# Performance work log

Hardware: AMD Instinct MI355X
Metric: run time of the kernel (lower is better)

## Reference

```python
import jax, jax.numpy as jnp
import numpy as np

N_NODES = 100000
N_EDGES = 1600000
EMB = 128
N_LAYER = 5
X_DIM = 178
E_DIM = 18
BN_EPS = 1e-5


def setup_inputs() -> dict:
    key = jax.random.key(0)
    ks = jax.random.split(key, 20)
    s = 0.05  # weight scale
    inp = {}
    inp["x"] = jax.random.normal(ks[0], (N_NODES, X_DIM), jnp.float32)
    inp["edge_attr"] = jax.random.uniform(ks[1], (N_EDGES, E_DIM), jnp.float32)
    # input MLP (178 -> emb -> emb, LeakyReLU 0.1)
    inp["iw1"] = jax.random.normal(ks[2], (X_DIM, EMB), jnp.float32) * s
    inp["ib1"] = jax.random.normal(ks[3], (EMB,), jnp.float32) * s
    inp["iw2"] = jax.random.normal(ks[4], (EMB, EMB), jnp.float32) * s
    inp["ib2"] = jax.random.normal(ks[5], (EMB,), jnp.float32) * s
    # per-layer edge embedding MLP (18 -> emb -> emb, LeakyReLU 0.1)
    inp["ew1"] = jax.random.normal(ks[6], (N_LAYER, E_DIM, EMB), jnp.float32) * s
    inp["eb1"] = jax.random.normal(ks[7], (N_LAYER, EMB), jnp.float32) * s
    inp["ew2"] = jax.random.normal(ks[8], (N_LAYER, EMB, EMB), jnp.float32) * s
    inp["eb2"] = jax.random.normal(ks[9], (N_LAYER, EMB), jnp.float32) * s
    # per-layer GIN update MLP (emb -> 2emb -> emb, ReLU)
    inp["mw1"] = jax.random.normal(ks[10], (N_LAYER, EMB, 2 * EMB), jnp.float32) * s
    inp["mb1"] = jax.random.normal(ks[11], (N_LAYER, 2 * EMB), jnp.float32) * s
    inp["mw2"] = jax.random.normal(ks[12], (N_LAYER, 2 * EMB, EMB), jnp.float32) * s
    inp["mb2"] = jax.random.normal(ks[13], (N_LAYER, EMB), jnp.float32) * s
    # per-layer BatchNorm affine params
    inp["gamma"] = jnp.ones((N_LAYER, EMB), jnp.float32)
    inp["beta"] = jnp.zeros((N_LAYER, EMB), jnp.float32)
    inp["edge_index"] = jax.random.randint(ks[14], (2, N_EDGES), 0, N_NODES)
    return inp


def _leaky(v):
    return jnp.where(v > 0, v, 0.1 * v)


def reference(x, edge_attr, iw1, ib1, iw2, ib2, ew1, eb1, ew2, eb2,
              mw1, mb1, mw2, mb2, gamma, beta, edge_index):
    src = edge_index[0]  # x_j gathered from source nodes (PyG source_to_target)
    dst = edge_index[1]
    n = x.shape[0]

    # input node MLP with LeakyReLU(0.1)
    h = _leaky(x @ iw1 + ib1) @ iw2 + ib2  # [N, EMB]

    for l in range(N_LAYER):
        # edge embeddings for real edges: [E, EMB]
        ee = _leaky(edge_attr @ ew1[l] + eb1[l]) @ ew2[l] + eb2[l]
        # self-loop edges have zero edge_attr -> constant embedding vector [EMB]
        self_e = _leaky(eb1[l]) @ ew2[l] + eb2[l]
        # message = x_j + edge_emb; aggregate (add) at destination, plus self-loop term
        msg = h[src] + ee
        aggr = jax.ops.segment_sum(msg, dst, num_segments=n) + h + self_e
        # GIN update MLP (ReLU)
        hh = jnp.maximum(aggr @ mw1[l] + mb1[l], 0.0) @ mw2[l] + mb2[l]
        # BatchNorm1d (training mode: batch stats, biased variance)
        mean = hh.mean(axis=0)
        var = hh.var(axis=0)
        hh = (hh - mean) / jnp.sqrt(var + BN_EPS) * gamma[l] + beta[l]
        if l < N_LAYER - 1:
            hh = jnp.maximum(hh, 0.0)  # ReLU on all but last layer; dropout p=0 is a no-op
        h = hh

    return h  # JK == 'last'
```

## Files before the change

### kernel.cpp

```cpp
#include <hip/hip_runtime.h>
#include <hip/hip_bf16.h>
#include <cstdint>
#include <cstddef>

#define NNODES 100000
#define NEDGES 1600000
#define EMBD 128
#define NLAYER 5
#define XDIM 178
#define EDIM 18
#define BNEPS 1e-5f

typedef __attribute__((ext_vector_type(8))) short short8;
typedef __attribute__((ext_vector_type(8))) unsigned short ushort8;
typedef __attribute__((ext_vector_type(4))) float f32x4;

static __device__ __forceinline__ float leakyf(float v){ return v > 0.f ? v : 0.1f*v; }
static __device__ __forceinline__ unsigned short f2b(float v){
  __hip_bfloat16 b = __float2bfloat16(v);
  return *reinterpret_cast<unsigned short*>(&b);
}
static __device__ __forceinline__ float b2f(unsigned short u){
  __hip_bfloat16 b = *reinterpret_cast<__hip_bfloat16*>(&u);
  return __bfloat162float(b);
}

__global__ __launch_bounds__(256) void k_hist(const int* __restrict__ dst, int* __restrict__ cnt){
  int e = blockIdx.x*256 + threadIdx.x;
  if (e < NEDGES) atomicAdd(&cnt[dst[e]], 1);
}

__global__ __launch_bounds__(256) void k_scan1(const int* __restrict__ cnt, int* __restrict__ rowptr,
                                               int* __restrict__ bsum){
  __shared__ int s[256];
  int t = threadIdx.x, i = blockIdx.x*256 + t;
  int v = (i < NNODES) ? cnt[i] : 0;
  s[t] = v; __syncthreads();
  for (int off=1; off<256; off<<=1){
    int x = (t>=off) ? s[t-off] : 0; __syncthreads();
    s[t] += x; __syncthreads();
  }
  if (i < NNODES) rowptr[i+1] = s[t];
  if (t == 255) bsum[blockIdx.x] = s[t];
}

__global__ __launch_bounds__(512) void k_scan2(const int* __restrict__ bsum, int* __restrict__ boff, int nb){
  __shared__ int s[512];
  int t = threadIdx.x;
  int v = (t < nb) ? bsum[t] : 0;
  s[t] = v; __syncthreads();
  for (int off=1; off<512; off<<=1){
    int x = (t>=off) ? s[t-off] : 0; __syncthreads();
    s[t] += x; __syncthreads();
  }
  if (t < nb) boff[t] = s[t] - v;
}

__global__ __launch_bounds__(256) void k_scan3(int* __restrict__ rowptr, const int* __restrict__ boff){
  int i = blockIdx.x*256 + threadIdx.x;
  if (i < NNODES) rowptr[i+1] += boff[i>>8];
  if (i == 0) rowptr[0] = 0;
}

__global__ __launch_bounds__(256) void k_curcopy(const int* __restrict__ rowptr, int* __restrict__ cursor){
  int i = blockIdx.x*256 + threadIdx.x;
  if (i < NNODES) cursor[i] = rowptr[i];
}

__global__ __launch_bounds__(256) void k_fill_new(const int* __restrict__ src, const int* __restrict__ dst,
                                                  const float* __restrict__ ea, int* __restrict__ cursor,
                                                  int* __restrict__ srcp, unsigned short* __restrict__ eap24){
  int e = blockIdx.x*256 + threadIdx.x;
  if (e >= NEDGES) return;
  int pos = atomicAdd(&cursor[dst[e]], 1);
  srcp[pos] = src[e];
  const float* a = ea + (size_t)e*EDIM;
  ushort8 r0, r1, r2;
  #pragma unroll
  for (int k=0;k<8;++k)  r0[k] = f2b(a[k]);
  #pragma unroll
  for (int k=0;k<8;++k)  r1[k] = f2b(a[8+k]);
  #pragma unroll
  for (int k=0;k<8;++k)  r2[k] = 0;
  r2[0] = f2b(a[16]); r2[1] = f2b(a[17]);
  r2[2] = 0x3F80;
  unsigned short* o = eap24 + (size_t)pos*24;
  *reinterpret_cast<ushort8*>(o)      = r0;
  *reinterpret_cast<ushort8*>(o + 8)  = r1;
  *reinterpret_cast<ushort8*>(o + 16) = r2;
}

__global__ __launch_bounds__(256) void k_fill(const int* __restrict__ src, const int* __restrict__ dst,
                                              const float* __restrict__ ea, int* __restrict__ cursor,
                                              int* __restrict__ perm, int* __restrict__ srcp,
                                              float* __restrict__ eap){
  int e = blockIdx.x*256 + threadIdx.x;
  if (e >= NEDGES) return;
  int pos = atomicAdd(&cursor[dst[e]], 1);
  perm[pos] = e;
  srcp[pos] = src[e];
  if (eap){
    const float* a = ea + (size_t)e*EDIM;
    float* o = eap + (size_t)pos*EDIM;
    #pragma unroll
    for (int k=0;k<EDIM;++k) o[k] = a[k];
  }
}

__global__ __launch_bounds__(128) void k_selfe(const float* __restrict__ eb1, const float* __restrict__ ew2,
                                               const float* __restrict__ eb2, float* __restrict__ selfe){
  int l = blockIdx.x, c = threadIdx.x;
  const float* b1 = eb1 + l*EMBD;
  const float* w2 = ew2 + (size_t)l*EMBD*EMBD;
  float acc = eb2[l*EMBD + c];
  for (int j=0;j<EMBD;++j) acc += leakyf(b1[j]) * w2[j*EMBD + c];
  selfe[l*EMBD + c] = acc;
}

__global__ __launch_bounds__(256) void k_wc(const float* __restrict__ ew2, const float* __restrict__ mw1,
                                            float* __restrict__ wc){
  int idx = blockIdx.x*256 + threadIdx.x;
  int l = idx >> 15, rem = idx & 32767;
  int i = rem >> 8, n = rem & 255;
  const float* e = ew2 + (size_t)l*EMBD*EMBD + i*EMBD;
  const float* m = mw1 + (size_t)l*EMBD*2*EMBD + n;
  float acc = 0.f;
  #pragma unroll 4
  for (int j=0;j<EMBD;++j) acc += e[j]*m[(size_t)j*2*EMBD];
  wc[idx] = acc;
}

__global__ __launch_bounds__(256) void k_pack(const float* __restrict__ s1, int rows1,
                                              const float* __restrict__ s2, int Kreal,
                                              int Kpad, int N, __hip_bfloat16* __restrict__ out){
  int idx = blockIdx.x*256 + threadIdx.x;
  if (idx >= Kpad*N) return;
  int k = idx / N, n = idx - k*N;
  float v = 0.f;
  if (k < rows1) v = s1[(size_t)k*N + n];
  else if (k < Kreal) v = s2[(size_t)(k-rows1)*N + n];
  unsigned short hi = f2b(v);
  unsigned short lo = f2b(v - b2f(hi));
  size_t o = (size_t)(k>>5)*N*32 + (size_t)n*32 + (k&31);
  unsigned short* po = (unsigned short*)out;
  po[o] = hi;
  po[(size_t)Kpad*N + o] = lo;
}

__global__ __launch_bounds__(256) void k_gather(
    const float* __restrict__ h, const int* __restrict__ rowptr,
    const int* __restrict__ srcp,
    const float* __restrict__ eb2l, const float* __restrict__ selfel,
    float* __restrict__ base)
{
  int tid = threadIdx.x;
  int li = tid & 31;
  int c4 = li*4;
  float4 sf4 = *(const float4*)(selfel + c4);
  float4 e24 = *(const float4*)(eb2l + c4);
  int slot = blockIdx.x*8 + (tid>>5);
  const int NS = gridDim.x*8;
  for (int node = slot; node < NNODES; node += NS){
    int rs = rowptr[node], re = rowptr[node+1];
    f32x4 b = (f32x4)0.f;
    for (int c0 = rs; c0 < re; c0 += 8){
      int cnt = re - c0;
      #pragma unroll
      for (int p=0;p<8;++p){
        int e = c0 + p; if (e > re-1) e = re-1;
        float m = (p < cnt) ? 1.f : 0.f;
        int sp = srcp[e];
        float4 hv = *(const float4*)(h + (size_t)sp*EMBD + c4);
        b[0] = fmaf(m, hv.x, b[0]);
        b[1] = fmaf(m, hv.y, b[1]);
        b[2] = fmaf(m, hv.z, b[2]);
        b[3] = fmaf(m, hv.w, b[3]);
      }
    }
    float deg = (float)(re - rs);
    float4 hn = *(const float4*)(h + (size_t)node*EMBD + c4);
    float4 o;
    o.x = b[0] + hn.x + sf4.x + deg*e24.x;
    o.y = b[1] + hn.y + sf4.y + deg*e24.y;
    o.z = b[2] + hn.z + sf4.z + deg*e24.z;
    o.w = b[3] + hn.w + sf4.w + deg*e24.w;
    *(float4*)(base + (size_t)node*EMBD + c4) = o;
  }
}

__global__ __launch_bounds__(256) void k_s1(
    const int* __restrict__ rowptr, const unsigned short* __restrict__ eap24,
    const float* __restrict__ ew1l, const float* __restrict__ eb1l,
    float* __restrict__ S1)
{
  int tid = threadIdx.x;
  int lane = tid & 63;
  int lr = lane & 15, kb = lane >> 4;

  short8 bh[8], bl[8];
  #pragma unroll
  for (int nf=0; nf<8; ++nf){
    int col = nf*16 + lr;
    ushort8 hh8, ll8;
    #pragma unroll
    for (int j=0;j<8;++j){
      int k = kb*8 + j;
      float v = 0.f;
      if (k < EDIM) v = ew1l[k*EMBD + col];
      else if (k == EDIM) v = eb1l[col];
      unsigned short hi = f2b(v);
      hh8[j] = hi;
      ll8[j] = f2b(v - b2f(hi));
    }
    bh[nf] = *reinterpret_cast<short8*>(&hh8);
    bl[nf] = *reinterpret_cast<short8*>(&ll8);
  }

  int wid = blockIdx.x*4 + (tid>>6);
  const int NW = gridDim.x*4;
  for (int node = wid; node < NNODES; node += NW){
    int rs = rowptr[node], re = rowptr[node+1];
    float s1p[8];
    #pragma unroll
    for (int nf=0;nf<8;++nf) s1p[nf]=0.f;

    for (int c0 = rs; c0 < re; c0 += 16){
      int cnt = re - c0;
      int idx = c0 + lr; if (idx > re-1) idx = re-1;
      short8 af = (short8)0;
      if (kb < 3){
        ushort8 t = *reinterpret_cast<const ushort8*>(eap24 + (size_t)idx*24 + kb*8);
        af = *reinterpret_cast<short8*>(&t);
      }
      if (lr >= cnt) af = (short8)0;
      #pragma unroll
      for (int nf=0;nf<8;++nf){
        f32x4 acc = (f32x4)0.f;
        acc = __builtin_amdgcn_mfma_f32_16x16x32_bf16(af, bl[nf], acc, 0,0,0);
        acc = __builtin_amdgcn_mfma_f32_16x16x32_bf16(af, bh[nf], acc, 0,0,0);
        #pragma unroll
        for (int j=0;j<4;++j){
          float v = acc[j];
          s1p[nf] = fmaf(0.55f, v, s1p[nf]);
          s1p[nf] = fmaf(0.45f, fabsf(v), s1p[nf]);
        }
      }
    }

    #pragma unroll
    for (int nf=0;nf<8;++nf){
      float v = s1p[nf];
      v += __shfl_xor(v, 16);
      v += __shfl_xor(v, 32);
      s1p[nf] = v;
    }
    float va = s1p[0], vb = s1p[1];
    if (kb == 1){ va = s1p[2]; vb = s1p[3]; }
    if (kb == 2){ va = s1p[4]; vb = s1p[5]; }
    if (kb == 3){ va = s1p[6]; vb = s1p[7]; }
    S1[(size_t)node*EMBD + kb*32 + lr]      = va;
    S1[(size_t)node*EMBD + kb*32 + 16 + lr] = vb;
  }
}

__global__ __launch_bounds__(256) void k_edge(
    const float* __restrict__ h, const int* __restrict__ rowptr,
    const int* __restrict__ perm, const int* __restrict__ srcp,
    const float* __restrict__ edge_attr, const float* __restrict__ eaperm,
    const float* __restrict__ ew1l, const float* __restrict__ eb1l,
    const float* __restrict__ eb2l, const float* __restrict__ selfel,
    float* __restrict__ S1, float* __restrict__ base)
{
  __shared__ float w1s[EDIM*EMBD];
  __shared__ float b1s[EMBD];
  int tid = threadIdx.x;
  for (int i = tid; i < EDIM*EMBD; i += 256) w1s[i] = ew1l[i];
  if (tid < EMBD) b1s[tid] = eb1l[tid];
  __syncthreads();
  int lane = tid & 63;
  int node = blockIdx.x*4 + (tid >> 6);
  if (node >= NNODES) return;
  int rs = rowptr[node], re = rowptr[node+1];
  int c0 = lane*2;
  float s1x=0.f, s1y=0.f, bx=0.f, by=0.f;
  for (int i = rs; i < re; ++i){
    int s = __builtin_amdgcn_readfirstlane(srcp[i]);
    const float* ea;
    if (eaperm){
      ea = eaperm + (size_t)__builtin_amdgcn_readfirstlane(i)*EDIM;
    } else {
      ea = edge_attr + (size_t)__builtin_amdgcn_readfirstlane(perm[i])*EDIM;
    }
    float2 hs = *(const float2*)(h + (size_t)s*EMBD + c0);
    bx += hs.x; by += hs.y;
    float d0 = b1s[c0], d1 = b1s[c0+1];
    #pragma unroll
    for (int k=0;k<EDIM;++k){
      float av = ea[k];
      d0 += av * w1s[k*EMBD + c0];
      d1 += av * w1s[k*EMBD + c0 + 1];
    }
    s1x += leakyf(d0); s1y += leakyf(d1);
  }
  float deg = (float)(re - rs);
  float2 hv = *(const float2*)(h + (size_t)node*EMBD + c0);
  *(float2*)(S1 + (size_t)node*EMBD + c0) = make_float2(s1x, s1y);
  float bvx = bx + hv.x + selfel[c0]   + deg*eb2l[c0];
  float bvy = by + hv.y + selfel[c0+1] + deg*eb2l[c0+1];
  *(float2*)(base + (size_t)node*EMBD + c0) = make_float2(bvx, bvy);
}

template<int BN, int WGM, int WGN, bool ALO, int ACT, bool STATS, bool OBF16, bool CONCAT, bool KCHK, bool ABF16>
__global__ __launch_bounds__(512) void k_mgemm(
    const float* __restrict__ Af, const float* __restrict__ A1,
    const __hip_bfloat16* __restrict__ Ab,
    int M, int Kreal, int Kpad, int lda,
    const __hip_bfloat16* __restrict__ Bp,
    const float* __restrict__ bias,
    float* __restrict__ Cf, __hip_bfloat16* __restrict__ Cb, int ldc,
    float* __restrict__ stats)
{
  static_assert(WGM*WGN == 8, "8 waves");
  constexpr int BM = 128;
  constexpr int MF = BM/(16*WGM);
  constexpr int NF = BN/(16*WGN);
  constexpr int LDS_ROW = 40;
  __shared__ __align__(16) unsigned short Ah[BM*LDS_ROW];
  __shared__ __align__(16) unsigned short Al[ALO ? BM*LDS_ROW : 8];
  __shared__ float ssum[STATS ? BN : 4];
  __shared__ float ssq [STATS ? BN : 4];

  int tid = threadIdx.x;
  int row0 = blockIdx.x*BM;
  int w = tid >> 6, lane = tid & 63;
  int wm = w / WGN, wn = w % WGN;
  int lr = lane & 15, kb = lane >> 4;
  int wrow = wm*MF*16, wcol = wn*NF*16;

  if (STATS && tid < BN){ ssum[tid] = 0.f; ssq[tid] = 0.f; }

  f32x4 acc[MF][NF];
  #pragma unroll
  for (int a=0;a<MF;++a)
    #pragma unroll
    for (int b=0;b<NF;++b) acc[a][b] = (f32x4)0.f;

  const size_t planeSz = (size_t)Kpad*BN;
  int sr = tid >> 2;
  int skq = (tid & 3)*8;
  int grow = row0 + sr;
  const int KS = Kpad >> 5;

  for (int ks = 0; ks < KS; ++ks){
    int k0 = ks << 5;
    int kg = k0 + skq;
    ushort8 hv, lv;
    if (ABF16){
      short8 raw = (short8)0;
      if (grow < M) raw = *reinterpret_cast<const short8*>((const unsigned short*)Ab + (size_t)grow*lda + kg);
      hv = *reinterpret_cast<ushort8*>(&raw);
    } else {
      float v[8];
      if (KCHK){
        #pragma unroll
        for (int i=0;i<8;++i)
          v[i] = (grow < M && kg+i < Kreal) ? Af[(size_t)grow*lda + kg + i] : 0.f;
      } else {
        const float* s;
        if (CONCAT) s = (kg < EMBD) ? (Af + (size_t)grow*lda + kg) : (A1 + (size_t)grow*lda + (kg - EMBD));
        else        s = Af + (size_t)grow*lda + kg;
        float4 p0 = make_float4(0,0,0,0), p1 = make_float4(0,0,0,0);
        if (grow < M){ p0 = *(const float4*)s; p1 = *(const float4*)(s+4); }
        v[0]=p0.x; v[1]=p0.y; v[2]=p0.z; v[3]=p0.w;
        v[4]=p1.x; v[5]=p1.y; v[6]=p1.z; v[7]=p1.w;
      }
      #pragma unroll
      for (int i=0;i<8;++i){
        unsigned short h16 = f2b(v[i]);
        hv[i] = h16;
        if (ALO) lv[i] = f2b(v[i] - b2f(h16));
      }
    }
    __syncthreads();
    *reinterpret_cast<ushort8*>(&Ah[sr*LDS_ROW + skq]) = hv;
    if (ALO && !ABF16) *reinterpret_cast<ushort8*>(&Al[sr*LDS_ROW + skq]) = lv;
    __syncthreads();

    short8 ah[MF], al[MF];
    #pragma unroll
    for (int mf=0; mf<MF; ++mf){
      int r = (wrow + mf*16 + lr)*LDS_ROW + kb*8;
      ah[mf] = *reinterpret_cast<const short8*>(&Ah[r]);
      if (ALO) al[mf] = *reinterpret_cast<const short8*>(&Al[r]);
    }
    const unsigned short* bb = (const unsigned short*)Bp + (size_t)ks*BN*32;
    short8 bh[NF], blv[NF];
    #pragma unroll
    for (int nf=0; nf<NF; ++nf){
      size_t off = (size_t)(wcol + nf*16 + lr)*32 + kb*8;
      bh[nf] = *reinterpret_cast<const short8*>(bb + off);
      blv[nf] = *reinterpret_cast<const short8*>(bb + planeSz + off);
    }
    #pragma unroll
    for (int mf=0; mf<MF; ++mf){
      #pragma unroll
      for (int nf=0; nf<NF; ++nf){
        acc[mf][nf] = __builtin_amdgcn_mfma_f32_16x16x32_bf16(ah[mf], bh[nf], acc[mf][nf], 0, 0, 0);
        acc[mf][nf] = __builtin_amdgcn_mfma_f32_16x16x32_bf16(ah[mf], blv[nf], acc[mf][nf], 0, 0, 0);
        if (ALO)
          acc[mf][nf] = __builtin_amdgcn_mfma_f32_16x16x32_bf16(al[mf], bh[nf], acc[mf][nf], 0, 0, 0);
      }
    }
  }

  float bcol[NF];
  #pragma unroll
  for (int nf=0; nf<NF; ++nf) bcol[nf] = bias ? bias[wcol + nf*16 + lr] : 0.f;
  float s[NF], sq[NF];
  #pragma unroll
  for (int nf=0; nf<NF; ++nf){ s[nf]=0.f; sq[nf]=0.f; }

  #pragma unroll
  for (int mf=0; mf<MF; ++mf){
    #pragma unroll
    for (int j=0; j<4; ++j){
      int r = row0 + wrow + mf*16 + kb*4 + j;
      if (r < M){
        #pragma unroll
        for (int nf=0; nf<NF; ++nf){
          int c = wcol + nf*16 + lr;
          float v = acc[mf][nf][j] + bcol[nf];
          if (ACT == 1) v = leakyf(v);
          if (ACT == 2) v = fmaxf(v, 0.f);
          if (OBF16) Cb[(size_t)r*ldc + c] = __float2bfloat16(v);
          else       Cf[(size_t)r*ldc + c] = v;
          if (STATS){ s[nf] += v; sq[nf] += v*v; }
        }
      }
    }
  }
  if (STATS){
    #pragma unroll
    for (int nf=0; nf<NF; ++nf){
      atomicAdd(&ssum[wcol + nf*16 + lr], s[nf]);
      atomicAdd(&ssq [wcol + nf*16 + lr], sq[nf]);
    }
    __syncthreads();
    if (tid < BN){
      atomicAdd(&stats[tid], ssum[tid]);
      atomicAdd(&stats[BN + tid], ssq[tid]);
    }
  }
}

__global__ __launch_bounds__(256) void k_bn(const float* __restrict__ hh, const float* __restrict__ stats,
                                            const float* __restrict__ gamma, const float* __restrict__ beta,
                                            float* __restrict__ out, int dorelu){
  int idx = blockIdx.x*256 + threadIdx.x;
  if (idx >= NNODES*(EMBD/4)) return;
  int c0 = (idx & (EMBD/4 - 1)) * 4;
  float4 v = *(const float4*)(hh + (size_t)idx*4);
  float o[4] = {v.x, v.y, v.z, v.w};
  const float invN = 1.f / (float)NNODES;
  #pragma unroll
  for (int i=0;i<4;++i){
    int c = c0 + i;
    float mean = stats[c] * invN;
    float var  = stats[EMBD + c] * invN - mean*mean;
    float inv  = rsqrtf(fmaxf(var, 0.f) + BNEPS);
    float y = (o[i] - mean) * inv * gamma[c] + beta[c];
    if (dorelu) y = fmaxf(y, 0.f);
    o[i] = y;
  }
  *(float4*)(out + (size_t)idx*4) = make_float4(o[0],o[1],o[2],o[3]);
}

extern "C" void kernel_launch(void* const* d_in, const int* in_sizes, int n_in,
                              void* d_out, int out_size, void* d_ws, size_t ws_size,
                              hipStream_t stream)
{
  const float* x   = (const float*)d_in[0];
  const float* ea  = (const float*)d_in[1];
  const float* iw1 = (const float*)d_in[2];
  const float* ib1 = (const float*)d_in[3];
  const float* iw2 = (const float*)d_in[4];
  const float* ib2 = (const float*)d_in[5];
  const float* ew1 = (const float*)d_in[6];
  const float* eb1 = (const float*)d_in[7];
  const float* ew2 = (const float*)d_in[8];
  const float* eb2 = (const float*)d_in[9];
  const float* mw1 = (const float*)d_in[10];
  const float* mb1 = (const float*)d_in[11];
  const float* mw2 = (const float*)d_in[12];
  const float* mb2 = (const float*)d_in[13];
  const float* gamma = (const float*)d_in[14];
  const float* beta  = (const float*)d_in[15];
  const int* eidx = (const int*)d_in[16];
  const int* srcI = eidx;
  const int* dstI = eidx + NEDGES;

  char* p = (char*)d_ws;
  auto alloc = [&](size_t bytes)->char*{
    char* r = p; p += (bytes + 255) & ~(size_t)255; return r;
  };
  float* hbuf  = (float*)alloc((size_t)NNODES*EMBD*4);
  float* S1    = (float*)alloc((size_t)NNODES*EMBD*4);
  float* base  = (float*)alloc((size_t)NNODES*EMBD*4);
  __hip_bfloat16* tbuf = (__hip_bfloat16*)alloc((size_t)NNODES*2*EMBD*2);
  int* perm   = (int*)alloc((size_t)NEDGES*4);
  int* srcp   = (int*)alloc((size_t)NEDGES*4);
  int* rowptr = (int*)alloc((size_t)(NNODES+1)*4);
  int* cursor = (int*)alloc((size_t)NNODES*4);
  int* bsum   = (int*)alloc(4096);
  int* boff   = (int*)alloc(4096);
  float* selfe = (float*)alloc(NLAYER*EMBD*4);
  float* stats = (float*)alloc(2*EMBD*4);
  float* wc    = (float*)alloc((size_t)NLAYER*EMBD*2*EMBD*4);
  __hip_bfloat16* Bi1 = (__hip_bfloat16*)alloc((size_t)192*EMBD*2*2);
  __hip_bfloat16* Bi2 = (__hip_bfloat16*)alloc((size_t)EMBD*EMBD*2*2);
  __hip_bfloat16* B1  = (__hip_bfloat16*)alloc((size_t)NLAYER*256*256*2*2);
  __hip_bfloat16* B2  = (__hip_bfloat16*)alloc((size_t)NLAYER*256*EMBD*2*2);
  size_t used = (size_t)(p - (char*)d_ws);

  bool use_new = (ws_size >= used + (size_t)NEDGES*24*2 + 256);
  unsigned short* eap24 = nullptr;
  float* eaperm = nullptr;
  if (use_new) eap24 = (unsigned short*)alloc((size_t)NEDGES*24*2);
  else if (ws_size >= used + (size_t)NEDGES*EDIM*4 + 256)
    eaperm = (float*)alloc((size_t)NEDGES*EDIM*4);

  hipMemsetAsync(cursor, 0, (size_t)NNODES*4, stream);
  k_hist<<<(NEDGES+255)/256, 256, 0, stream>>>(dstI, cursor);
  int nb = (NNODES+255)/256;
  k_scan1<<<nb, 256, 0, stream>>>(cursor, rowptr, bsum);
  k_scan2<<<1, 512, 0, stream>>>(bsum, boff, nb);
  k_scan3<<<(NNODES+255)/256, 256, 0, stream>>>(rowptr, boff);
  k_curcopy<<<(NNODES+255)/256, 256, 0, stream>>>(rowptr, cursor);
  if (use_new)
    k_fill_new<<<(NEDGES+255)/256, 256, 0, stream>>>(srcI, dstI, ea, cursor, srcp, eap24);
  else
    k_fill<<<(NEDGES+255)/256, 256, 0, stream>>>(srcI, dstI, ea, cursor, perm, srcp, eaperm);
  k_selfe<<<NLAYER, EMBD, 0, stream>>>(eb1, ew2, eb2, selfe);

  k_wc<<<(NLAYER*EMBD*2*EMBD)/256, 256, 0, stream>>>(ew2, mw1, wc);
  k_pack<<<(192*EMBD+255)/256, 256, 0, stream>>>(iw1, XDIM, iw1, XDIM, 192, EMBD, Bi1);
  k_pack<<<(EMBD*EMBD+255)/256, 256, 0, stream>>>(iw2, EMBD, iw2, EMBD, EMBD, EMBD, Bi2);
  for (int l=0; l<NLAYER; ++l){
    k_pack<<<(256*256+255)/256, 256, 0, stream>>>(
        wc + (size_t)l*EMBD*2*EMBD, EMBD, mw1 + (size_t)l*EMBD*2*EMBD, 256, 256, 256,
        B1 + (size_t)l*256*256*2);
    k_pack<<<(256*EMBD+255)/256, 256, 0, stream>>>(
        mw2 + (size_t)l*2*EMBD*EMBD, 256, mw2, 256, 256, EMBD,
        B2 + (size_t)l*256*EMBD*2);
  }

  const int gx = (NNODES + 127)/128;

  k_mgemm<128,4,2, true,1,false,false,false,true ,false><<<gx, 512, 0, stream>>>(
      x, nullptr, nullptr, NNODES, XDIM, 192, XDIM, Bi1, ib1, S1, nullptr, EMBD, nullptr);
  k_mgemm<128,4,2, true,0,false,false,false,false,false><<<gx, 512, 0, stream>>>(
      S1, nullptr, nullptr, NNODES, EMBD, EMBD, EMBD, Bi2, ib2, hbuf, nullptr, EMBD, nullptr);

  for (int l=0; l<NLAYER; ++l){
    hipMemsetAsync(stats, 0, 2*EMBD*4, stream);
    if (use_new){
      k_gather<<<2048, 256, 0, stream>>>(
          hbuf, rowptr, srcp, eb2 + l*EMBD, selfe + l*EMBD, base);
      k_s1<<<2048, 256, 0, stream>>>(
          rowptr, eap24, ew1 + (size_t)l*EDIM*EMBD, eb1 + l*EMBD, S1);
    } else {
      k_edge<<<NNODES/4, 256, 0, stream>>>(
          hbuf, rowptr, perm, srcp, ea, eaperm,
          ew1 + (size_t)l*EDIM*EMBD, eb1 + l*EMBD, eb2 + l*EMBD, selfe + l*EMBD,
          S1, base);
    }
    k_mgemm<256,2,4, true,2,false,true ,true ,false,false><<<gx, 512, 0, stream>>>(
        S1, base, nullptr, NNODES, 256, 256, EMBD, B1 + (size_t)l*256*256*2,
        mb1 + l*2*EMBD, nullptr, tbuf, 2*EMBD, nullptr);
    k_mgemm<128,4,2, false,0,true ,false,false,false,true ><<<gx, 512, 0, stream>>>(
        nullptr, nullptr, tbuf, NNODES, 256, 256, 2*EMBD, B2 + (size_t)l*256*EMBD*2,
        mb2 + l*EMBD, S1, nullptr, EMBD, stats);
    float* outp = (l == NLAYER-1) ? (float*)d_out : hbuf;
    k_bn<<<(NNODES*(EMBD/4)+255)/256, 256, 0, stream>>>(
        S1, stats, gamma + l*EMBD, beta + l*EMBD, outp, (l < NLAYER-1) ? 1 : 0);
  }
}
```

Measured before the change: 2.239 ms.

## Gather neighbor features from fp16 copy and interleave two nodes in edge-MLP kernel

Adds an fp16 shadow copy of the node features, written by the input GEMM and BatchNorm epilogues, and a gather kernel that reads neighbor rows from it. This halves the bytes fetched in the random-access neighbor sum. Separately, the edge-embedding MFMA kernel now processes two nodes per wave at once to expose more independent loads and MFMAs, with a min-occupancy launch bound and half the grid. The fp16 gather adds rounding error to the message sum, and the extra fp16 writes add traffic in the producer kernels.

```diff
diff --git a/kernel.cpp b/kernel.cpp
--- a/kernel.cpp
+++ b/kernel.cpp
@@ -1,5 +1,6 @@
 #include <hip/hip_runtime.h>
 #include <hip/hip_bf16.h>
+#include <hip/hip_fp16.h>
 #include <cstdint>
 #include <cstddef>
 
@@ -23,6 +24,14 @@
 static __device__ __forceinline__ float b2f(unsigned short u){
   __hip_bfloat16 b = *reinterpret_cast<__hip_bfloat16*>(&u);
   return __bfloat162float(b);
+}
+static __device__ __forceinline__ unsigned short f2h(float v){
+  __half h = __float2half(v);
+  return *reinterpret_cast<unsigned short*>(&h);
+}
+static __device__ __forceinline__ float h2f(unsigned short u){
+  __half h = *reinterpret_cast<__half*>(&u);
+  return __half2float(h);
 }
 
 __global__ __launch_bounds__(256) void k_hist(const int* __restrict__ dst, int* __restrict__ cnt){
@@ -145,6 +154,47 @@
   unsigned short* po = (unsigned short*)out;
   po[o] = hi;
   po[(size_t)Kpad*N + o] = lo;
+}
+
+__global__ __launch_bounds__(256) void k_gather_h(
+    const float* __restrict__ h, const unsigned short* __restrict__ hh,
+    const int* __restrict__ rowptr, const int* __restrict__ srcp,
+    const float* __restrict__ eb2l, const float* __restrict__ selfel,
+    float* __restrict__ base)
+{
+  int tid = threadIdx.x;
+  int li = tid & 31;
+  int c4 = li*4;
+  float4 sf4 = *(const float4*)(selfel + c4);
+  float4 e24 = *(const float4*)(eb2l + c4);
+  int slot = blockIdx.x*8 + (tid>>5);
+  const int NS = gridDim.x*8;
+  for (int node = slot; node < NNODES; node += NS){
+    int rs = rowptr[node], re = rowptr[node+1];
+    f32x4 b = (f32x4)0.f;
+    for (int c0 = rs; c0 < re; c0 += 8){
+      int cnt = re - c0;
+      #pragma unroll
+      for (int p=0;p<8;++p){
+        int e = c0 + p; if (e > re-1) e = re-1;
+        float m = (p < cnt) ? 1.f : 0.f;
+        int sp = srcp[e];
+        uint2 hv = *(const uint2*)(hh + (size_t)sp*EMBD + c4);
+        b[0] = fmaf(m, h2f((unsigned short)(hv.x & 0xffffu)), b[0]);
+        b[1] = fmaf(m, h2f((unsigned short)(hv.x >> 16)),     b[1]);
+        b[2] = fmaf(m, h2f((unsigned short)(hv.y & 0xffffu)), b[2]);
+        b[3] = fmaf(m, h2f((unsigned short)(hv.y >> 16)),     b[3]);
+      }
+    }
+    float deg = (float)(re - rs);
+    float4 hn = *(const float4*)(h + (size_t)node*EMBD + c4);
+    float4 o;
+    o.x = b[0] + hn.x + sf4.x + deg*e24.x;
+    o.y = b[1] + hn.y + sf4.y + deg*e24.y;
+    o.z = b[2] + hn.z + sf4.z + deg*e24.z;
+    o.w = b[3] + hn.w + sf4.w + deg*e24.w;
+    *(float4*)(base + (size_t)node*EMBD + c4) = o;
+  }
 }
 
 __global__ __launch_bounds__(256) void k_gather(
@@ -188,7 +238,7 @@
   }
 }
 
-__global__ __launch_bounds__(256) void k_s1(
+__global__ __launch_bounds__(256, 4) void k_s1(
     const int* __restrict__ rowptr, const unsigned short* __restrict__ eap24,
     const float* __restrict__ ew1l, const float* __restrict__ eb1l,
     float* __restrict__ S1)
@@ -216,50 +266,96 @@
     bl[nf] = *reinterpret_cast<short8*>(&ll8);
   }
 
+  auto loadC = [&](int c0, int re)->short8{
+    int cnt = re - c0;
+    int idx = c0 + lr; if (idx > re-1) idx = re-1;
+    short8 af = (short8)0;
+    if (kb < 3){
+      ushort8 t = *reinterpret_cast<const ushort8*>(eap24 + (size_t)idx*24 + kb*8);
+      af = *reinterpret_cast<short8*>(&t);
+    }
+    if (lr >= cnt) af = (short8)0;
+    return af;
+  };
+
   int wid = blockIdx.x*4 + (tid>>6);
   const int NW = gridDim.x*4;
-  for (int node = wid; node < NNODES; node += NW){
-    int rs = rowptr[node], re = rowptr[node+1];
-    float s1p[8];
-    #pragma unroll
-    for (int nf=0;nf<8;++nf) s1p[nf]=0.f;
-
-    for (int c0 = rs; c0 < re; c0 += 16){
-      int cnt = re - c0;
-      int idx = c0 + lr; if (idx > re-1) idx = re-1;
-      short8 af = (short8)0;
-      if (kb < 3){
-        ushort8 t = *reinterpret_cast<const ushort8*>(eap24 + (size_t)idx*24 + kb*8);
-        af = *reinterpret_cast<short8*>(&t);
-      }
-      if (lr >= cnt) af = (short8)0;
+  for (int nA = wid; nA < NNODES; nA += 2*NW){
+    int nB = nA + NW;
+    bool hasB = (nB < NNODES);
+    int rsA = rowptr[nA], reA = rowptr[nA+1];
+    int rsB = 0, reB = 0;
+    if (hasB){ rsB = rowptr[nB]; reB = rowptr[nB+1]; }
+    float sA[8], sB[8];
+    #pragma unroll
+    for (int nf=0;nf<8;++nf){ sA[nf]=0.f; sB[nf]=0.f; }
+    int cA = rsA, cB = rsB;
+    while (cA < reA || cB < reB){
+      bool dA = cA < reA, dB = cB < reB;
+      short8 afA = (short8)0, afB = (short8)0;
+      if (dA) afA = loadC(cA, reA);
+      if (dB) afB = loadC(cB, reB);
+      if (dA){
+        #pragma unroll
+        for (int nf=0;nf<8;++nf){
+          f32x4 acc = (f32x4)0.f;
+          acc = __builtin_amdgcn_mfma_f32_16x16x32_bf16(afA, bl[nf], acc, 0,0,0);
+          acc = __builtin_amdgcn_mfma_f32_16x16x32_bf16(afA, bh[nf], acc, 0,0,0);
+          #pragma unroll
+          for (int j=0;j<4;++j){
+            float v = acc[j];
+            sA[nf] = fmaf(0.55f, v, sA[nf]);
+            sA[nf] = fmaf(0.45f, fabsf(v), sA[nf]);
+          }
+        }
+      }
+      if (dB){
+        #pragma unroll
+        for (int nf=0;nf<8;++nf){
+          f32x4 acc = (f32x4)0.f;
+          acc = __builtin_amdgcn_mfma_f32_16x16x32_bf16(afB, bl[nf], acc, 0,0,0);
+          acc = __builtin_amdgcn_mfma_f32_16x16x32_bf16(afB, bh[nf], acc, 0,0,0);
+          #pragma unroll
+          for (int j=0;j<4;++j){
+            float v = acc[j];
+            sB[nf] = fmaf(0.55f, v, sB[nf]);
+            sB[nf] = fmaf(0.45f, fabsf(v), sB[nf]);
+          }
+        }
+      }
+      cA += 16; cB += 16;
+    }
+
+    {
       #pragma unroll
       for (int nf=0;nf<8;++nf){
-        f32x4 acc = (f32x4)0.f;
-        acc = __builtin_amdgcn_mfma_f32_16x16x32_bf16(af, bl[nf], acc, 0,0,0);
-        acc = __builtin_amdgcn_mfma_f32_16x16x32_bf16(af, bh[nf], acc, 0,0,0);
-        #pragma unroll
-        for (int j=0;j<4;++j){
-          float v = acc[j];
-          s1p[nf] = fmaf(0.55f, v, s1p[nf]);
-          s1p[nf] = fmaf(0.45f, fabsf(v), s1p[nf]);
-        }
-      }
-    }
-
-    #pragma unroll
-    for (int nf=0;nf<8;++nf){
-      float v = s1p[nf];
-      v += __shfl_xor(v, 16);
-      v += __shfl_xor(v, 32);
-      s1p[nf] = v;
-    }
-    float va = s1p[0], vb = s1p[1];
-    if (kb == 1){ va = s1p[2]; vb = s1p[3]; }
-    if (kb == 2){ va = s1p[4]; vb = s1p[5]; }
-    if (kb == 3){ va = s1p[6]; vb = s1p[7]; }
-    S1[(size_t)node*EMBD + kb*32 + lr]      = va;
-    S1[(size_t)node*EMBD + kb*32 + 16 + lr] = vb;
+        float v = sA[nf];
+        v += __shfl_xor(v, 16);
+        v += __shfl_xor(v, 32);
+        sA[nf] = v;
+      }
+      float va = sA[0], vb = sA[1];
+      if (kb == 1){ va = sA[2]; vb = sA[3]; }
+      if (kb == 2){ va = sA[4]; vb = sA[5]; }
+      if (kb == 3){ va = sA[6]; vb = sA[7]; }
+      S1[(size_t)nA*EMBD + kb*32 + lr]      = va;
+      S1[(size_t)nA*EMBD + kb*32 + 16 + lr] = vb;
+    }
+    if (hasB){
+      #pragma unroll
+      for (int nf=0;nf<8;++nf){
+        float v = sB[nf];
+        v += __shfl_xor(v, 16);
+        v += __shfl_xor(v, 32);
+        sB[nf] = v;
+      }
+      float va = sB[0], vb = sB[1];
+      if (kb == 1){ va = sB[2]; vb = sB[3]; }
+      if (kb == 2){ va = sB[4]; vb = sB[5]; }
+      if (kb == 3){ va = sB[6]; vb = sB[7]; }
+      S1[(size_t)nB*EMBD + kb*32 + lr]      = va;
+      S1[(size_t)nB*EMBD + kb*32 + 16 + lr] = vb;
+    }
   }
 }
 
@@ -318,7 +414,7 @@
     const __hip_bfloat16* __restrict__ Bp,
     const float* __restrict__ bias,
     float* __restrict__ Cf, __hip_bfloat16* __restrict__ Cb, int ldc,
-    float* __restrict__ stats)
+    float* __restrict__ stats, unsigned short* __restrict__ Ch)
 {
   static_assert(WGM*WGN == 8, "8 waves");
   constexpr int BM = 128;
@@ -434,6 +530,7 @@
           if (ACT == 2) v = fmaxf(v, 0.f);
           if (OBF16) Cb[(size_t)r*ldc + c] = __float2bfloat16(v);
           else       Cf[(size_t)r*ldc + c] = v;
+          if (Ch) Ch[(size_t)r*ldc + c] = f2h(v);
           if (STATS){ s[nf] += v; sq[nf] += v*v; }
         }
       }
@@ -455,7 +552,8 @@
 
 __global__ __launch_bounds__(256) void k_bn(const float* __restrict__ hh, const float* __restrict__ stats,
                                             const float* __restrict__ gamma, const float* __restrict__ beta,
-                                            float* __restrict__ out, int dorelu){
+                                            float* __restrict__ out, unsigned short* __restrict__ outh,
+                                            int dorelu){
   int idx = blockIdx.x*256 + threadIdx.x;
   if (idx >= NNODES*(EMBD/4)) return;
   int c0 = (idx & (EMBD/4 - 1)) * 4;
@@ -473,6 +571,15 @@
     o[i] = y;
   }
   *(float4*)(out + (size_t)idx*4) = make_float4(o[0],o[1],o[2],o[3]);
+  if (outh){
+    ushort8 dummy;
+    unsigned short p0 = f2h(o[0]), p1 = f2h(o[1]), p2 = f2h(o[2]), p3 = f2h(o[3]);
+    uint2 pk;
+    pk.x = (unsigned)p0 | ((unsigned)p1 << 16);
+    pk.y = (unsigned)p2 | ((unsigned)p3 << 16);
+    *reinterpret_cast<uint2*>(outh + (size_t)idx*4) = pk;
+    (void)dummy;
+  }
 }
 
 extern "C" void kernel_launch(void* const* d_in, const int* in_sizes, int n_in,
@@ -529,6 +636,11 @@
   else if (ws_size >= used + (size_t)NEDGES*EDIM*4 + 256)
     eaperm = (float*)alloc((size_t)NEDGES*EDIM*4);
 
+  used = (size_t)(p - (char*)d_ws);
+  bool use_h16 = use_new && (ws_size >= used + (size_t)NNODES*EMBD*2 + 256);
+  unsigned short* hh16 = nullptr;
+  if (use_h16) hh16 = (unsigned short*)alloc((size_t)NNODES*EMBD*2);
+
   hipMemsetAsync(cursor, 0, (size_t)NNODES*4, stream);
   k_hist<<<(NEDGES+255)/256, 256, 0, stream>>>(dstI, cursor);
   int nb = (NNODES+255)/256;
@@ -557,16 +669,21 @@
   const int gx = (NNODES + 127)/128;
 
   k_mgemm<128,4,2, true,1,false,false,false,true ,false><<<gx, 512, 0, stream>>>(
-      x, nullptr, nullptr, NNODES, XDIM, 192, XDIM, Bi1, ib1, S1, nullptr, EMBD, nullptr);
+      x, nullptr, nullptr, NNODES, XDIM, 192, XDIM, Bi1, ib1, S1, nullptr, EMBD, nullptr, nullptr);
   k_mgemm<128,4,2, true,0,false,false,false,false,false><<<gx, 512, 0, stream>>>(
-      S1, nullptr, nullptr, NNODES, EMBD, EMBD, EMBD, Bi2, ib2, hbuf, nullptr, EMBD, nullptr);
+      S1, nullptr, nullptr, NNODES, EMBD, EMBD, EMBD, Bi2, ib2, hbuf, nullptr, EMBD, nullptr,
+      use_h16 ? hh16 : nullptr);
 
   for (int l=0; l<NLAYER; ++l){
     hipMemsetAsync(stats, 0, 2*EMBD*4, stream);
     if (use_new){
-      k_gather<<<2048, 256, 0, stream>>>(
-          hbuf, rowptr, srcp, eb2 + l*EMBD, selfe + l*EMBD, base);
-      k_s1<<<2048, 256, 0, stream>>>(
+      if (use_h16)
+        k_gather_h<<<2048, 256, 0, stream>>>(
+            hbuf, hh16, rowptr, srcp, eb2 + l*EMBD, selfe + l*EMBD, base);
+      else
+        k_gather<<<2048, 256, 0, stream>>>(
+            hbuf, rowptr, srcp, eb2 + l*EMBD, selfe + l*EMBD, base);
+      k_s1<<<1024, 256, 0, stream>>>(
           rowptr, eap24, ew1 + (size_t)l*EDIM*EMBD, eb1 + l*EMBD, S1);
     } else {
       k_edge<<<NNODES/4, 256, 0, stream>>>(
@@ -576,12 +693,13 @@
     }
     k_mgemm<256,2,4, true,2,false,true ,true ,false,false><<<gx, 512, 0, stream>>>(
         S1, base, nullptr, NNODES, 256, 256, EMBD, B1 + (size_t)l*256*256*2,
-        mb1 + l*2*EMBD, nullptr, tbuf, 2*EMBD, nullptr);
+        mb1 + l*2*EMBD, nullptr, tbuf, 2*EMBD, nullptr, nullptr);
     k_mgemm<128,4,2, false,0,true ,false,false,false,true ><<<gx, 512, 0, stream>>>(
         nullptr, nullptr, tbuf, NNODES, 256, 256, 2*EMBD, B2 + (size_t)l*256*EMBD*2,
-        mb2 + l*EMBD, S1, nullptr, EMBD, stats);
+        mb2 + l*EMBD, S1, nullptr, EMBD, stats, nullptr);
     float* outp = (l == NLAYER-1) ? (float*)d_out : hbuf;
+    unsigned short* outh = (l < NLAYER-1 && use_h16) ? hh16 : nullptr;
     k_bn<<<(NNODES*(EMBD/4)+255)/256, 256, 0, stream>>>(
-        S1, stats, gamma + l*EMBD, beta + l*EMBD, outp, (l < NLAYER-1) ? 1 : 0);
-  }
-}
+        S1, stats, gamma + l*EMBD, beta + l*EMBD, outp, outh, (l < NLAYER-1) ? 1 : 0);
+  }
+}
```

New measurement: 2.021 ms. -9.7%, faster.
